# Optimization experiments

Hardware: AMD Instinct MI355X
Metric: run time of the kernel (lower is better)

The kernel has to match this reference:

```python
import jax, jax.numpy as jnp
import numpy as np

N_QUBITS = 16
DEPTH = 4
BATCH = 512

# Convention: wire 0 is the most-significant bit of the state index (PennyLane default).

def _rx(t):
    # t: scalar or (B,) real angle -> (2,2) or (B,2,2) complex RX matrix
    h = 0.5 * t
    c = jnp.cos(h).astype(jnp.complex64)
    s = (-1j * jnp.sin(h)).astype(jnp.complex64)
    return jnp.stack([jnp.stack([c, s], -1), jnp.stack([s, c], -1)], -2)

def _ry(t):
    h = 0.5 * t
    c = jnp.cos(h).astype(jnp.complex64)
    s = jnp.sin(h).astype(jnp.complex64)
    return jnp.stack([jnp.stack([c, -s], -1), jnp.stack([s, c], -1)], -2)

def _rz(t):
    e = jnp.exp(-0.5j * t.astype(jnp.complex64))  # diag(e^{-it/2}, e^{+it/2})
    z = jnp.zeros_like(e)
    return jnp.stack([jnp.stack([e, z], -1), jnp.stack([z, jnp.conj(e)], -1)], -2)

def _apply_1q(state, U, q, n):
    # state: (B, 2^n); U: (2,2) shared or (B,2,2) per-batch
    B = state.shape[0]
    L, R = 2 ** q, 2 ** (n - q - 1)
    s = state.reshape(B, L, 2, R)
    if U.ndim == 2:
        s = jnp.einsum('ij,bljr->blir', U, s)
    else:
        s = jnp.einsum('bij,bljr->blir', U, s)
    return s.reshape(B, -1)

def _apply_cnot(state, c, t, n):
    # flips target bit t where control bit c == 1
    B = state.shape[0]
    a, b = min(c, t), max(c, t)
    s = state.reshape(B, 2 ** a, 2, 2 ** (b - a - 1), 2, 2 ** (n - b - 1))
    if c < t:
        # control axis=2, target axis=4
        s1 = s[:, :, 1]                      # (B, 2^a, mid, 2, rest)
        flipped = s1[:, :, :, ::-1, :]
        s = jnp.stack([s[:, :, 0], flipped], axis=2)
    else:
        # control axis=4, target axis=2
        s1 = s[:, :, :, :, 1, :]             # (B, 2^a, 2, mid, rest)
        flipped = s1[:, :, ::-1]
        s = jnp.stack([s[:, :, :, :, 0, :], flipped], axis=4)
    return s.reshape(B, -1)

def _circuit(x, params):
    B, n = x.shape
    depth = params.shape[0]
    state = jnp.zeros((B, 2 ** n), jnp.complex64).at[:, 0].set(1.0)
    # data encoding: batched RX per wire
    for i in range(n):
        state = _apply_1q(state, _rx(x[:, i]), i, n)
    for layer in range(depth):
        for i in range(n):
            # circuit applies RZ then RX then RY -> fuse into one 2x2 matrix
            U = _ry(params[layer, i, 2]) @ _rx(params[layer, i, 1]) @ _rz(params[layer, i, 0])
            state = _apply_1q(state, U, i, n)
        for i in range(n - 1):
            state = _apply_cnot(state, i, i + 1, n)
        state = _apply_cnot(state, n - 1, 0, n)
    # <Z_i> = P(bit_i = 0) - P(bit_i = 1)
    probs = state.real ** 2 + state.imag ** 2
    expz = []
    for i in range(n):
        p = probs.reshape(B, 2 ** i, 2, 2 ** (n - i - 1))
        expz.append(p[:, :, 0].sum((1, 2)) - p[:, :, 1].sum((1, 2)))
    return jnp.stack(expz, axis=1)  # (B, n_qubits)


def setup_inputs() -> dict:
    key = jax.random.key(0)
    k1, k2 = jax.random.split(key)
    x = jax.random.normal(k1, (BATCH, N_QUBITS), dtype=jnp.float32)
    params = jax.random.normal(k2, (DEPTH, N_QUBITS, 3), dtype=jnp.float32)
    return {"x": x, "params": params}


def reference(x, params):
    return _circuit(x, params)
```

## Files before the change

kernel.cpp:

```cpp
#include <hip/hip_runtime.h>


#define NQ 16
#define TPB 256

typedef float __attribute__((ext_vector_type(2))) f2;

__device__ __forceinline__ f2 f2s(float s) { return (f2){s, s}; }

__device__ __forceinline__ f2 cmulpk(f2 a, f2 b) {
    f2 bs = { -b.y, b.x };
    f2 r = f2s(a.x) * b;
    return __builtin_elementwise_fma(f2s(a.y), bs, r);
}

__device__ __forceinline__ void computeU(const float* params, int layer, int q, f2* U) {
    const float* p = params + (layer*NQ + q)*3;
    float s0, c0, s1, c1, s2, c2;
    sincosf(0.5f*p[0], &s0, &c0);
    sincosf(0.5f*p[1], &s1, &c1);
    sincosf(0.5f*p[2], &s2, &c2);
    f2 m00 = { c1*c0, -c1*s0};
    f2 m01 = { s1*s0, -s1*c0};
    f2 m10 = {-s1*s0, -s1*c0};
    f2 m11 = { c1*c0,  c1*s0};
    U[0] = c2*m00 - s2*m10;
    U[1] = c2*m01 - s2*m11;
    U[2] = s2*m00 + c2*m10;
    U[3] = s2*m01 + c2*m11;
}

template<int MASK, int N>
__device__ __forceinline__ void gateN(f2* A, f2 u00, f2 u01, f2 u10, f2 u11) {
    #pragma unroll
    for (int a = 0; a < N; ++a) {
        if (!(a & MASK)) {
            f2 x = A[a], y = A[a | MASK];
            f2 xs = { -x.y, x.x };
            f2 ys = { -y.y, y.x };
            f2 nx = f2s(u00.x) * x;
            nx = __builtin_elementwise_fma(f2s(u00.y), xs, nx);
            nx = __builtin_elementwise_fma(f2s(u01.x), y,  nx);
            nx = __builtin_elementwise_fma(f2s(u01.y), ys, nx);
            f2 ny = f2s(u10.x) * x;
            ny = __builtin_elementwise_fma(f2s(u10.y), xs, ny);
            ny = __builtin_elementwise_fma(f2s(u11.x), y,  ny);
            ny = __builtin_elementwise_fma(f2s(u11.y), ys, ny);
            A[a] = nx; A[a | MASK] = ny;
        }
    }
}
template<int MASK> __device__ __forceinline__ void gate32(f2* A, f2 a, f2 b, f2 c, f2 d) { gateN<MASK,32>(A,a,b,c,d); }
template<int MASK> __device__ __forceinline__ void gate16(f2* A, f2 a, f2 b, f2 c, f2 d) { gateN<MASK,16>(A,a,b,c,d); }

__device__ __forceinline__ constexpr int permB(int ad) {
    return (ad & 1)
         | ((((ad >> 1) ^ (ad >> 2)) & 1) << 1)
         | ((((ad >> 2) ^ (ad >> 3)) & 1) << 2)
         | ((((ad >> 3) ^ (ad >> 4)) & 1) << 3)
         | ((((ad >> 4) ^  ad      ) & 1) << 4);
}

__device__ __forceinline__ void transpose_1to3(f2* A, f2* S, int t) {
    #pragma unroll
    for (int h = 0; h < 2; ++h) {
        __syncthreads();
        #pragma unroll
        for (int c = 0; c < 8; ++c) {
            int slot = ((t << 1) | (c << 9)) ^ (((t >> 4) & 7) << 1);
            f2 a0 = A[h*16 + 2*c], a1 = A[h*16 + 2*c + 1];
            *(float4*)&S[slot] = make_float4(a0.x, a0.y, a1.x, a1.y);
        }
        __syncthreads();
        #pragma unroll
        for (int rr = 0; rr < 16; ++rr) {
            int jj = (t & 31) | (rr << 5) | (((t >> 5) & 7) << 9);
            A[h*16 + rr] = S[jj ^ ((rr & 7) << 1)];
        }
    }
}

__device__ __forceinline__ void transpose_1to2(f2* A, f2* S, int t) {
    #pragma unroll
    for (int h = 0; h < 2; ++h) {
        __syncthreads();
        #pragma unroll
        for (int c = 0; c < 8; ++c) {
            int slot = ((t << 1) | (c << 9)) ^ (((t >> 4) & 7) << 1);
            f2 a0 = A[h*16 + 2*c], a1 = A[h*16 + 2*c + 1];
            *(float4*)&S[slot] = make_float4(a0.x, a0.y, a1.x, a1.y);
        }
        __syncthreads();
        #pragma unroll
        for (int rr = 0; rr < 16; ++rr) {
            int jj = (t & 1) | (rr << 1) | (((t >> 1) & 15) << 5) | (((t >> 5) & 7) << 9);
            A[h*16 + rr] = S[jj ^ (((t >> 1) & 7) << 1)];
        }
    }
}

__device__ __forceinline__ void transpose_2to3(f2* A, f2* S, int t) {
    #pragma unroll
    for (int h = 0; h < 2; ++h) {
        __syncthreads();
        #pragma unroll
        for (int rr = 0; rr < 16; ++rr) {
            int jj = (t & 1) | (rr << 1) | (((t >> 1) & 15) << 5) | (((t >> 5) & 7) << 9);
            S[jj ^ (((t >> 1) & 7) << 1)] = A[h*16 + rr];
        }
        __syncthreads();
        #pragma unroll
        for (int rr = 0; rr < 16; ++rr) {
            int jj = (t & 31) | (rr << 5) | (((t >> 5) & 7) << 9);
            A[h*16 + rr] = S[jj ^ ((rr & 7) << 1)];
        }
    }
}

__device__ __forceinline__ int b_qb(int tt) { return (tt < 3) ? (15 - tt) : (10 - tt); }
__device__ __forceinline__ int a_qb(int tt) { return (tt == 0) ? 12 : (tt < 5) ? (4 - tt) : (16 - tt); }
__device__ __forceinline__ int bf_qb(int tt) {
    return (tt == 0) ? 12 : (tt == 1) ? 0 : (tt < 5) ? (17 - tt) : (16 - tt);
}

__global__ __launch_bounds__(TPB, 4) void qc_B1_gen(
    const float* __restrict__ x, const float* __restrict__ params,
    f2* __restrict__ st)
{
    __shared__ __align__(16) f2 S[4096];
    __shared__ f2 Ush[7][4];
    __shared__ f2 V[16][2];

    const int t    = threadIdx.x;
    const int b    = blockIdx.x >> 3;
    const int fixb = blockIdx.x & 7;
    f2* base = st + ((size_t)b << NQ);

    if (t < 16) {
        f2 U[4];
        computeU(params, 0, t, U);
        float s, c;
        sincosf(0.5f * x[b*NQ + t], &s, &c);
        V[15 - t][0] = (f2){U[0].x*c + U[1].y*s, U[0].y*c - U[1].x*s};
        V[15 - t][1] = (f2){U[2].x*c + U[3].y*s, U[2].y*c - U[3].x*s};
    } else if (t < 23) {
        int tt = t - 16;
        computeU(params, 1, b_qb(tt), Ush[tt]);
    }
    __syncthreads();

    const int f0 = fixb & 1, f1 = (fixb >> 1) & 1, f2b = (fixb >> 2) & 1;
    const int t0 = t & 1,  t7 = (t >> 7) & 1;

    f2 pre = V[4][(t ^ (t >> 1)) & 1];
    #pragma unroll
    for (int bb = 5; bb <= 10; ++bb)
        pre = cmulpk(pre, V[bb][((t >> (bb - 4)) ^ (t >> (bb - 3))) & 1]);
    pre = cmulpk(pre, V[11][t7 ^ f0]);
    pre = cmulpk(pre, V[12][f0 ^ f1]);
    pre = cmulpk(pre, V[13][f1 ^ f2b]);

    f2 P0 = cmulpk(pre, V[3][t0]);
    f2 P1 = cmulpk(pre, V[3][1 ^ t0]);
    f2 Q[4];
    Q[0] = cmulpk(P0, V[2][0]); Q[1] = cmulpk(P1, V[2][0]);
    Q[2] = cmulpk(P0, V[2][1]); Q[3] = cmulpk(P1, V[2][1]);
    f2 Rr[4];
    Rr[0] = cmulpk(V[0][0], V[1][0]); Rr[1] = cmulpk(V[0][1], V[1][0]);
    Rr[2] = cmulpk(V[0][0], V[1][1]); Rr[3] = cmulpk(V[0][1], V[1][1]);
    f2 G0 = cmulpk(V[15][0], V[14][f2b]);
    f2 G1 = cmulpk(V[15][1], V[14][1 ^ f2b]);
    f2 TT[8];
    #pragma unroll
    for (int e = 0; e < 4; ++e) {
        TT[2*e]     = cmulpk(G0, Rr[e]);
        TT[2*e + 1] = cmulpk(G1, Rr[e]);
    }

    f2 A[32];
    #pragma unroll
    for (int a = 0; a < 32; ++a) {
        const int a0 = a & 1;
        const int e1 = ((a >> 1) ^ (a >> 2)) & 1;
        const int e2 = ((a >> 2) ^ (a >> 3)) & 1;
        const int e3 = ((a >> 3) ^ (a >> 4)) & 1;
        const int e4 = ((a >> 4) ^  a      ) & 1;
        A[a] = cmulpk(Q[a0 + 2*e4], TT[e1 + 2*e2 + 4*e3]);
    }

    gate32<4> (A, Ush[0][0], Ush[0][1], Ush[0][2], Ush[0][3]);
    gate32<8> (A, Ush[1][0], Ush[1][1], Ush[1][2], Ush[1][3]);
    gate32<16>(A, Ush[2][0], Ush[2][1], Ush[2][2], Ush[2][3]);

    transpose_1to3(A, S, t);
    gate32<1>(A, Ush[3][0], Ush[3][1], Ush[3][2], Ush[3][3]);
    gate32<2>(A, Ush[4][0], Ush[4][1], Ush[4][2], Ush[4][3]);
    gate32<4>(A, Ush[5][0], Ush[5][1], Ush[5][2], Ush[5][3]);
    gate32<8>(A, Ush[6][0], Ush[6][1], Ush[6][2], Ush[6][3]);

    #pragma unroll
    for (int h = 0; h < 2; ++h) {
        #pragma unroll
        for (int rr = 0; rr < 16; ++rr) {
            int d = (t & 31) | (rr << 5) | (((t >> 5) & 7) << 9) | (h << 12);
            int m = (d & 511) | (fixb << 9) | (((d >> 9) & 1) << 12) | ((d >> 10) << 13);
            base[m] = A[h*16 + rr];
        }
    }
}

__global__ __launch_bounds__(TPB, 4) void qc_B_heavy(
    const float* __restrict__ params, f2* __restrict__ st, int lm)
{
    __shared__ __align__(16) f2 S[4096];
    __shared__ f2 Ush[7][4];

    const int t    = threadIdx.x;
    const int b    = blockIdx.x >> 3;
    const int fixb = blockIdx.x & 7;
    f2* base = st + ((size_t)b << NQ);

    if (t < 7) computeU(params, lm, b_qb(t), Ush[t]);

    f2 R[32];
    #pragma unroll
    for (int k = 0; k < 16; ++k) {
        int j = 2*(t + 256*k);
        int m = (j & 511) | (fixb << 9) | (((j >> 9) & 1) << 12) | ((j >> 10) << 13);
        float4 v = *(const float4*)(base + m);
        R[2*k]   = (f2){v.x, v.y};
        R[2*k+1] = (f2){v.z, v.w};
    }
    f2 A[32];
    #pragma unroll
    for (int a = 0; a < 32; ++a) A[a] = R[permB(a)];
    __syncthreads();

    gate32<4> (A, Ush[0][0], Ush[0][1], Ush[0][2], Ush[0][3]);
    gate32<8> (A, Ush[1][0], Ush[1][1], Ush[1][2], Ush[1][3]);
    gate32<16>(A, Ush[2][0], Ush[2][1], Ush[2][2], Ush[2][3]);

    transpose_1to3(A, S, t);
    gate32<1>(A, Ush[3][0], Ush[3][1], Ush[3][2], Ush[3][3]);
    gate32<2>(A, Ush[4][0], Ush[4][1], Ush[4][2], Ush[4][3]);
    gate32<4>(A, Ush[5][0], Ush[5][1], Ush[5][2], Ush[5][3]);
    gate32<8>(A, Ush[6][0], Ush[6][1], Ush[6][2], Ush[6][3]);

    #pragma unroll
    for (int h = 0; h < 2; ++h) {
        #pragma unroll
        for (int rr = 0; rr < 16; ++rr) {
            int d = (t & 31) | (rr << 5) | (((t >> 5) & 7) << 9) | (h << 12);
            int m = (d & 511) | (fixb << 9) | (((d >> 9) & 1) << 12) | ((d >> 10) << 13);
            base[m] = A[h*16 + rr];
        }
    }
}

__global__ __launch_bounds__(TPB, 4) void qc_A_lite(
    const float* __restrict__ params, f2* __restrict__ st, int layer, int stealL)
{
    __shared__ __align__(16) f2 S[4096];
    __shared__ f2 Ush[9][4];
    __shared__ f2 Uq[3][4];
    const int t    = threadIdx.x;
    const int b    = blockIdx.x >> 3;
    const int fix3 = blockIdx.x & 7;
    f2* base = st + ((size_t)b << NQ) + (fix3 << 13);

    if (t < 9) computeU(params, layer, a_qb(t), Ush[t]);
    if (stealL >= 0 && t >= 16 && t < 19)
        computeU(params, stealL, 3 - (t - 16), Uq[t - 16]);

    f2 A[32];
    const float4* src = (const float4*)base;
    #pragma unroll
    for (int k = 0; k < 16; ++k) {
        float4 v = src[t + 256*k];
        A[2*k]   = (f2){v.x, v.y};
        A[2*k+1] = (f2){v.z, v.w};
    }
    __syncthreads();

    gate32<1> (A, Ush[0][0], Ush[0][1], Ush[0][2], Ush[0][3]);
    gate32<2> (A, Ush[1][0], Ush[1][1], Ush[1][2], Ush[1][3]);
    gate32<4> (A, Ush[2][0], Ush[2][1], Ush[2][2], Ush[2][3]);
    gate32<8> (A, Ush[3][0], Ush[3][1], Ush[3][2], Ush[3][3]);
    gate32<16>(A, Ush[4][0], Ush[4][1], Ush[4][2], Ush[4][3]);

    transpose_1to2(A, S, t);
    gate32<1>(A, Ush[5][0], Ush[5][1], Ush[5][2], Ush[5][3]);
    gate32<2>(A, Ush[6][0], Ush[6][1], Ush[6][2], Ush[6][3]);
    gate32<4>(A, Ush[7][0], Ush[7][1], Ush[7][2], Ush[7][3]);
    gate32<8>(A, Ush[8][0], Ush[8][1], Ush[8][2], Ush[8][3]);

    float4* dst = (float4*)base;
    #pragma unroll
    for (int h = 0; h < 2; ++h) {
        __syncthreads();
        #pragma unroll
        for (int rr = 0; rr < 16; ++rr) {
            int jj = (t & 1) | (rr << 1) | (((t >> 1) & 15) << 5) | (((t >> 5) & 7) << 9);
            S[jj ^ (((t >> 1) & 7) << 1)] = A[h*16 + rr];
        }
        __syncthreads();
        #pragma unroll
        for (int k = 0; k < 8; ++k) {
            int d  = 2*(t + 256*k);
            int i0 = d ^ (d >> 1) ^ (h << 11);
            int i1 = (d+1) ^ ((d+1) >> 1) ^ (h << 11);
            A[h*16 + 2*k]     = S[i0 ^ (((i0 >> 5) & 7) << 1)];
            A[h*16 + 2*k + 1] = S[i1 ^ (((i1 >> 5) & 7) << 1)];
        }
        if (stealL >= 0) {
            gate16<2>(&A[h*16], Uq[0][0], Uq[0][1], Uq[0][2], Uq[0][3]);
            gate16<4>(&A[h*16], Uq[1][0], Uq[1][1], Uq[1][2], Uq[1][3]);
            gate16<8>(&A[h*16], Uq[2][0], Uq[2][1], Uq[2][2], Uq[2][3]);
        }
        #pragma unroll
        for (int k = 0; k < 8; ++k) {
            f2 a0 = A[h*16 + 2*k], a1 = A[h*16 + 2*k + 1];
            dst[(t + 256*k) | (h << 11)] = make_float4(a0.x, a0.y, a1.x, a1.y);
        }
    }
}

__global__ __launch_bounds__(TPB, 4) void qc_B_final(
    const float* __restrict__ params, const f2* __restrict__ st,
    float* __restrict__ out)
{
    __shared__ __align__(16) f2 S[4096];
    __shared__ f2 Ush[13][4];
    float* F = (float*)S;

    const int t    = threadIdx.x;
    const int b    = blockIdx.x >> 3;
    const int fixb = blockIdx.x & 7;
    const f2* base = st + ((size_t)b << NQ);

    if (t < 13) computeU(params, 3, bf_qb(t), Ush[t]);

    f2 R[32];
    #pragma unroll
    for (int k = 0; k < 16; ++k) {
        int j = 2*(t + 256*k);
        int m = (j & 511) | (fixb << 9) | (((j >> 9) & 1) << 12) | ((j >> 10) << 13);
        float4 v = *(const float4*)(base + m);
        R[2*k]   = (f2){v.x, v.y};
        R[2*k+1] = (f2){v.z, v.w};
    }
    f2 A[32];
    #pragma unroll
    for (int a = 0; a < 32; ++a) A[a] = R[permB(a)];
    __syncthreads();

    gate32<1> (A, Ush[0][0],  Ush[0][1],  Ush[0][2],  Ush[0][3]);
    gate32<2> (A, Ush[1][0],  Ush[1][1],  Ush[1][2],  Ush[1][3]);
    gate32<4> (A, Ush[2][0],  Ush[2][1],  Ush[2][2],  Ush[2][3]);
    gate32<8> (A, Ush[3][0],  Ush[3][1],  Ush[3][2],  Ush[3][3]);
    gate32<16>(A, Ush[4][0],  Ush[4][1],  Ush[4][2],  Ush[4][3]);

    transpose_1to2(A, S, t);
    gate32<1>(A, Ush[5][0], Ush[5][1], Ush[5][2], Ush[5][3]);
    gate32<2>(A, Ush[6][0], Ush[6][1], Ush[6][2], Ush[6][3]);
    gate32<4>(A, Ush[7][0], Ush[7][1], Ush[7][2], Ush[7][3]);
    gate32<8>(A, Ush[8][0], Ush[8][1], Ush[8][2], Ush[8][3]);

    transpose_2to3(A, S, t);
    gate32<1>(A, Ush[9][0],  Ush[9][1],  Ush[9][2],  Ush[9][3]);
    gate32<2>(A, Ush[10][0], Ush[10][1], Ush[10][2], Ush[10][3]);
    gate32<4>(A, Ush[11][0], Ush[11][1], Ush[11][2], Ush[11][3]);
    gate32<8>(A, Ush[12][0], Ush[12][1], Ush[12][2], Ush[12][3]);

    float M0 = 0.f, M1 = 0.f, M2 = 0.f, M3 = 0.f, M4 = 0.f, M5 = 0.f;
    #pragma unroll
    for (int h = 0; h < 2; ++h) {
        #pragma unroll
        for (int rr = 0; rr < 16; ++rr) {
            f2 v = A[h*16 + rr];
            float p = v.x*v.x + v.y*v.y;
            M0 += p;
            M1 += (__popc(rr)      & 1) ? -p : p;
            M2 += (__popc(rr >> 1) & 1) ? -p : p;
            M3 += (__popc(rr >> 2) & 1) ? -p : p;
            M4 += (rr >> 3)             ? -p : p;
            M5 += ((__popc(rr) ^ h) & 1) ? -p : p;
        }
    }

    const int pf   = __popc(fixb) & 1;
    const int t5b  = (t >> 5) & 1, t6b = (t >> 6) & 1, t7b = (t >> 7) & 1;
    const int pt04 = __popc(t & 31) & 1;
    const int bs   = pf ^ t5b;

    float acc[NQ];
    acc[0]  = ((t6b ^ t7b ^ pt04 ^ pf) & 1) ? -M5 : M5;
    acc[1]  = (((fixb >> 2) ^ t5b) & 1)      ? -M0 : M0;
    acc[2]  = ((__popc(fixb >> 1) ^ t5b) & 1)? -M0 : M0;
    acc[3]  = (bs & 1)                        ? -M0 : M0;
    acc[4]  = (bs & 1)                        ? -M4 : M4;
    acc[5]  = (bs & 1)                        ? -M3 : M3;
    acc[6]  = (bs & 1)                        ? -M2 : M2;
    acc[7]  = (bs & 1)                        ? -M1 : M1;
    acc[8]  = ((((t >> 4) & 1) ^ bs) & 1)     ? -M1 : M1;
    acc[9]  = ((__popc((t >> 3) & 3)  ^ bs) & 1) ? -M1 : M1;
    acc[10] = ((__popc((t >> 2) & 7)  ^ bs) & 1) ? -M1 : M1;
    acc[11] = ((__popc((t >> 1) & 15) ^ bs) & 1) ? -M1 : M1;
    acc[12] = ((pt04 ^ bs) & 1)               ? -M1 : M1;
    acc[13] = ((pt04 ^ bs) & 1)               ? -M5 : M5;
    acc[14] = ((t7b ^ pt04 ^ bs) & 1)         ? -M5 : M5;
    acc[15] = ((t6b ^ t7b ^ pt04 ^ bs) & 1)   ? -M5 : M5;

    __syncthreads();
    #pragma unroll
    for (int q = 0; q < NQ; ++q) F[q*272 + t] = acc[q];
    __syncthreads();
    const int qq = t >> 4, ii = t & 15;
    float s = 0.f;
    #pragma unroll
    for (int c = 0; c < 16; ++c) s += F[qq*272 + ii + 16*c];
    s += __shfl_down(s, 8, 16);
    s += __shfl_down(s, 4, 16);
    s += __shfl_down(s, 2, 16);
    s += __shfl_down(s, 1, 16);
    if (ii == 0) atomicAdd(&out[b*NQ + qq], s);
}

extern "C" void kernel_launch(void* const* d_in, const int* in_sizes, int n_in,
                              void* d_out, int out_size, void* d_ws, size_t ws_size,
                              hipStream_t stream)
{
    (void)in_sizes; (void)n_in; (void)ws_size;
    const float* x      = (const float*)d_in[0];
    const float* params = (const float*)d_in[1];
    float* out = (float*)d_out;
    f2* st = (f2*)d_ws;

    hipMemsetAsync(d_out, 0, (size_t)out_size * sizeof(float), stream);
    qc_B1_gen <<<dim3(512*8), dim3(TPB), 0, stream>>>(x, params, st);
    qc_A_lite <<<dim3(512*8), dim3(TPB), 0, stream>>>(params, st, 1, -1);
    qc_B_heavy<<<dim3(512*8), dim3(TPB), 0, stream>>>(params, st, 2);
    qc_A_lite <<<dim3(512*8), dim3(TPB), 0, stream>>>(params, st, 2, 3);
    qc_B_final<<<dim3(512*8), dim3(TPB), 0, stream>>>(params, st, out);
}
```

Baseline: 574.2 us.

## Rebalance gate work: move qubit gates into B_heavy, simplify steal kernel transposes

B_heavy now applies 11 gates per pass, using two transposes (1to2, then 2to3) instead of one, and absorbs gates that were previously done in the second A pass. A new qc_A_steal kernel applies only 5 layer gates, then does a plain transpose and applies the three stolen next-layer gates. Those gates act in a CNOT-permuted basis through a new gateR pair-selection helper, which avoids the Gray-code shuffle before the gates. The aim is to cut per-kernel shared-memory transpose and sync overhead and balance arithmetic across passes, at the cost of an extra transpose in B_heavy.

```diff
diff --git a/kernel.cpp b/kernel.cpp
--- a/kernel.cpp
+++ b/kernel.cpp
@@ -30,28 +30,34 @@
     U[3] = s2*m01 + c2*m11;
 }
 
-template<int MASK, int N>
-__device__ __forceinline__ void gateN(f2* A, f2 u00, f2 u01, f2 u10, f2 u11) {
-    #pragma unroll
-    for (int a = 0; a < N; ++a) {
-        if (!(a & MASK)) {
-            f2 x = A[a], y = A[a | MASK];
-            f2 xs = { -x.y, x.x };
-            f2 ys = { -y.y, y.x };
-            f2 nx = f2s(u00.x) * x;
-            nx = __builtin_elementwise_fma(f2s(u00.y), xs, nx);
-            nx = __builtin_elementwise_fma(f2s(u01.x), y,  nx);
-            nx = __builtin_elementwise_fma(f2s(u01.y), ys, nx);
-            f2 ny = f2s(u10.x) * x;
-            ny = __builtin_elementwise_fma(f2s(u10.y), xs, ny);
-            ny = __builtin_elementwise_fma(f2s(u11.x), y,  ny);
-            ny = __builtin_elementwise_fma(f2s(u11.y), ys, ny);
-            A[a] = nx; A[a | MASK] = ny;
-        }
-    }
-}
-template<int MASK> __device__ __forceinline__ void gate32(f2* A, f2 a, f2 b, f2 c, f2 d) { gateN<MASK,32>(A,a,b,c,d); }
-template<int MASK> __device__ __forceinline__ void gate16(f2* A, f2 a, f2 b, f2 c, f2 d) { gateN<MASK,16>(A,a,b,c,d); }
+__device__ __forceinline__ void cpair(f2& X, f2& Y, f2 u00, f2 u01, f2 u10, f2 u11) {
+    f2 x = X, y = Y;
+    f2 xs = { -x.y, x.x };
+    f2 ys = { -y.y, y.x };
+    f2 nx = f2s(u00.x) * x;
+    nx = __builtin_elementwise_fma(f2s(u00.y), xs, nx);
+    nx = __builtin_elementwise_fma(f2s(u01.x), y,  nx);
+    nx = __builtin_elementwise_fma(f2s(u01.y), ys, nx);
+    f2 ny = f2s(u10.x) * x;
+    ny = __builtin_elementwise_fma(f2s(u10.y), xs, ny);
+    ny = __builtin_elementwise_fma(f2s(u11.x), y,  ny);
+    ny = __builtin_elementwise_fma(f2s(u11.y), ys, ny);
+    X = nx; Y = ny;
+}
+
+template<int MASK>
+__device__ __forceinline__ void gate32(f2* A, f2 u00, f2 u01, f2 u10, f2 u11) {
+    #pragma unroll
+    for (int a = 0; a < 32; ++a)
+        if (!(a & MASK)) cpair(A[a], A[a | MASK], u00, u01, u10, u11);
+}
+
+template<int MASK, int RM>
+__device__ __forceinline__ void gateR(f2* A, f2 u00, f2 u01, f2 u10, f2 u11) {
+    #pragma unroll
+    for (int a = 0; a < 32; ++a)
+        if ((__popc(a & RM) & 1) == 0) cpair(A[a], A[a ^ MASK], u00, u01, u10, u11);
+}
 
 __device__ __forceinline__ constexpr int permB(int ad) {
     return (ad & 1)
@@ -119,6 +125,7 @@
 
 __device__ __forceinline__ int b_qb(int tt) { return (tt < 3) ? (15 - tt) : (10 - tt); }
 __device__ __forceinline__ int a_qb(int tt) { return (tt == 0) ? 12 : (tt < 5) ? (4 - tt) : (16 - tt); }
+__device__ __forceinline__ int bh_qb(int tt) { return (tt < 3) ? (15 - tt) : (14 - tt); }
 __device__ __forceinline__ int bf_qb(int tt) {
     return (tt == 0) ? 12 : (tt == 1) ? 0 : (tt < 5) ? (17 - tt) : (16 - tt);
 }
@@ -213,14 +220,14 @@
     const float* __restrict__ params, f2* __restrict__ st, int lm)
 {
     __shared__ __align__(16) f2 S[4096];
-    __shared__ f2 Ush[7][4];
+    __shared__ f2 Ush[11][4];
 
     const int t    = threadIdx.x;
     const int b    = blockIdx.x >> 3;
     const int fixb = blockIdx.x & 7;
     f2* base = st + ((size_t)b << NQ);
 
-    if (t < 7) computeU(params, lm, b_qb(t), Ush[t]);
+    if (t < 11) computeU(params, lm, bh_qb(t), Ush[t]);
 
     f2 R[32];
     #pragma unroll
@@ -240,12 +247,18 @@
     gate32<8> (A, Ush[1][0], Ush[1][1], Ush[1][2], Ush[1][3]);
     gate32<16>(A, Ush[2][0], Ush[2][1], Ush[2][2], Ush[2][3]);
 
-    transpose_1to3(A, S, t);
+    transpose_1to2(A, S, t);
     gate32<1>(A, Ush[3][0], Ush[3][1], Ush[3][2], Ush[3][3]);
     gate32<2>(A, Ush[4][0], Ush[4][1], Ush[4][2], Ush[4][3]);
     gate32<4>(A, Ush[5][0], Ush[5][1], Ush[5][2], Ush[5][3]);
     gate32<8>(A, Ush[6][0], Ush[6][1], Ush[6][2], Ush[6][3]);
 
+    transpose_2to3(A, S, t);
+    gate32<1>(A, Ush[7][0],  Ush[7][1],  Ush[7][2],  Ush[7][3]);
+    gate32<2>(A, Ush[8][0],  Ush[8][1],  Ush[8][2],  Ush[8][3]);
+    gate32<4>(A, Ush[9][0],  Ush[9][1],  Ush[9][2],  Ush[9][3]);
+    gate32<8>(A, Ush[10][0], Ush[10][1], Ush[10][2], Ush[10][3]);
+
     #pragma unroll
     for (int h = 0; h < 2; ++h) {
         #pragma unroll
@@ -258,19 +271,74 @@
 }
 
 __global__ __launch_bounds__(TPB, 4) void qc_A_lite(
+    const float* __restrict__ params, f2* __restrict__ st, int layer)
+{
+    __shared__ __align__(16) f2 S[4096];
+    __shared__ f2 Ush[9][4];
+    const int t    = threadIdx.x;
+    const int b    = blockIdx.x >> 3;
+    const int fix3 = blockIdx.x & 7;
+    f2* base = st + ((size_t)b << NQ) + (fix3 << 13);
+
+    if (t < 9) computeU(params, layer, a_qb(t), Ush[t]);
+
+    f2 A[32];
+    const float4* src = (const float4*)base;
+    #pragma unroll
+    for (int k = 0; k < 16; ++k) {
+        float4 v = src[t + 256*k];
+        A[2*k]   = (f2){v.x, v.y};
+        A[2*k+1] = (f2){v.z, v.w};
+    }
+    __syncthreads();
+
+    gate32<1> (A, Ush[0][0], Ush[0][1], Ush[0][2], Ush[0][3]);
+    gate32<2> (A, Ush[1][0], Ush[1][1], Ush[1][2], Ush[1][3]);
+    gate32<4> (A, Ush[2][0], Ush[2][1], Ush[2][2], Ush[2][3]);
+    gate32<8> (A, Ush[3][0], Ush[3][1], Ush[3][2], Ush[3][3]);
+    gate32<16>(A, Ush[4][0], Ush[4][1], Ush[4][2], Ush[4][3]);
+
+    transpose_1to2(A, S, t);
+    gate32<1>(A, Ush[5][0], Ush[5][1], Ush[5][2], Ush[5][3]);
+    gate32<2>(A, Ush[6][0], Ush[6][1], Ush[6][2], Ush[6][3]);
+    gate32<4>(A, Ush[7][0], Ush[7][1], Ush[7][2], Ush[7][3]);
+    gate32<8>(A, Ush[8][0], Ush[8][1], Ush[8][2], Ush[8][3]);
+
+    float4* dst = (float4*)base;
+    #pragma unroll
+    for (int h = 0; h < 2; ++h) {
+        __syncthreads();
+        #pragma unroll
+        for (int rr = 0; rr < 16; ++rr) {
+            int jj = (t & 1) | (rr << 1) | (((t >> 1) & 15) << 5) | (((t >> 5) & 7) << 9);
+            S[jj ^ (((t >> 1) & 7) << 1)] = A[h*16 + rr];
+        }
+        __syncthreads();
+        #pragma unroll
+        for (int k = 0; k < 8; ++k) {
+            int d  = 2*(t + 256*k);
+            int i0 = d ^ (d >> 1) ^ (h << 11);
+            int i1 = (d+1) ^ ((d+1) >> 1) ^ (h << 11);
+            f2 a0 = S[i0 ^ (((i0 >> 5) & 7) << 1)];
+            f2 a1 = S[i1 ^ (((i1 >> 5) & 7) << 1)];
+            dst[(t + 256*k) | (h << 11)] = make_float4(a0.x, a0.y, a1.x, a1.y);
+        }
+    }
+}
+
+__global__ __launch_bounds__(TPB, 4) void qc_A_steal(
     const float* __restrict__ params, f2* __restrict__ st, int layer, int stealL)
 {
     __shared__ __align__(16) f2 S[4096];
-    __shared__ f2 Ush[9][4];
+    __shared__ f2 Ush[5][4];
     __shared__ f2 Uq[3][4];
     const int t    = threadIdx.x;
     const int b    = blockIdx.x >> 3;
     const int fix3 = blockIdx.x & 7;
     f2* base = st + ((size_t)b << NQ) + (fix3 << 13);
 
-    if (t < 9) computeU(params, layer, a_qb(t), Ush[t]);
-    if (stealL >= 0 && t >= 16 && t < 19)
-        computeU(params, stealL, 3 - (t - 16), Uq[t - 16]);
+    if (t < 5) computeU(params, layer, (t == 0) ? 12 : 4 - t, Ush[t]);
+    if (t >= 16 && t < 19) computeU(params, stealL, 3 - (t - 16), Uq[t - 16]);
 
     f2 A[32];
     const float4* src = (const float4*)base;
@@ -288,11 +356,26 @@
     gate32<8> (A, Ush[3][0], Ush[3][1], Ush[3][2], Ush[3][3]);
     gate32<16>(A, Ush[4][0], Ush[4][1], Ush[4][2], Ush[4][3]);
 
-    transpose_1to2(A, S, t);
-    gate32<1>(A, Ush[5][0], Ush[5][1], Ush[5][2], Ush[5][3]);
-    gate32<2>(A, Ush[6][0], Ush[6][1], Ush[6][2], Ush[6][3]);
-    gate32<4>(A, Ush[7][0], Ush[7][1], Ush[7][2], Ush[7][3]);
-    gate32<8>(A, Ush[8][0], Ush[8][1], Ush[8][2], Ush[8][3]);
+    #pragma unroll
+    for (int h = 0; h < 2; ++h) {
+        __syncthreads();
+        #pragma unroll
+        for (int c = 0; c < 8; ++c) {
+            int slot = ((t << 1) | (c << 9)) ^ (((t >> 4) & 7) << 1);
+            f2 a0 = A[h*16 + 2*c], a1 = A[h*16 + 2*c + 1];
+            *(float4*)&S[slot] = make_float4(a0.x, a0.y, a1.x, a1.y);
+        }
+        __syncthreads();
+        #pragma unroll
+        for (int rr = 0; rr < 16; ++rr) {
+            int idx = t | (rr << 8);
+            A[h*16 + rr] = S[idx ^ (((idx >> 5) & 7) << 1)];
+        }
+    }
+
+    gateR<3, 30>(A, Uq[0][0], Uq[0][1], Uq[0][2], Uq[0][3]);
+    gateR<6, 28>(A, Uq[1][0], Uq[1][1], Uq[1][2], Uq[1][3]);
+    gateR<12,24>(A, Uq[2][0], Uq[2][1], Uq[2][2], Uq[2][3]);
 
     float4* dst = (float4*)base;
     #pragma unroll
@@ -300,8 +383,8 @@
         __syncthreads();
         #pragma unroll
         for (int rr = 0; rr < 16; ++rr) {
-            int jj = (t & 1) | (rr << 1) | (((t >> 1) & 15) << 5) | (((t >> 5) & 7) << 9);
-            S[jj ^ (((t >> 1) & 7) << 1)] = A[h*16 + rr];
+            int idx = t | (rr << 8);
+            S[idx ^ (((idx >> 5) & 7) << 1)] = A[h*16 + rr];
         }
         __syncthreads();
         #pragma unroll
@@ -309,17 +392,8 @@
             int d  = 2*(t + 256*k);
             int i0 = d ^ (d >> 1) ^ (h << 11);
             int i1 = (d+1) ^ ((d+1) >> 1) ^ (h << 11);
-            A[h*16 + 2*k]     = S[i0 ^ (((i0 >> 5) & 7) << 1)];
-            A[h*16 + 2*k + 1] = S[i1 ^ (((i1 >> 5) & 7) << 1)];
-        }
-        if (stealL >= 0) {
-            gate16<2>(&A[h*16], Uq[0][0], Uq[0][1], Uq[0][2], Uq[0][3]);
-            gate16<4>(&A[h*16], Uq[1][0], Uq[1][1], Uq[1][2], Uq[1][3]);
-            gate16<8>(&A[h*16], Uq[2][0], Uq[2][1], Uq[2][2], Uq[2][3]);
-        }
-        #pragma unroll
-        for (int k = 0; k < 8; ++k) {
-            f2 a0 = A[h*16 + 2*k], a1 = A[h*16 + 2*k + 1];
+            f2 a0 = S[i0 ^ (((i0 >> 5) & 7) << 1)];
+            f2 a1 = S[i1 ^ (((i1 >> 5) & 7) << 1)];
             dst[(t + 256*k) | (h << 11)] = make_float4(a0.x, a0.y, a1.x, a1.y);
         }
     }
@@ -438,8 +512,8 @@
 
     hipMemsetAsync(d_out, 0, (size_t)out_size * sizeof(float), stream);
     qc_B1_gen <<<dim3(512*8), dim3(TPB), 0, stream>>>(x, params, st);
-    qc_A_lite <<<dim3(512*8), dim3(TPB), 0, stream>>>(params, st, 1, -1);
+    qc_A_lite <<<dim3(512*8), dim3(TPB), 0, stream>>>(params, st, 1);
     qc_B_heavy<<<dim3(512*8), dim3(TPB), 0, stream>>>(params, st, 2);
-    qc_A_lite <<<dim3(512*8), dim3(TPB), 0, stream>>>(params, st, 2, 3);
+    qc_A_steal<<<dim3(512*8), dim3(TPB), 0, stream>>>(params, st, 2, 3);
     qc_B_final<<<dim3(512*8), dim3(TPB), 0, stream>>>(params, st, out);
 }
```

After: 509.5 us. 11.3% less time.
